# Kernel tuning notes

Hardware: AMD Instinct MI355X
Metric: run time of the kernel (lower is better)

The kernel has to match this reference:

```python
import jax, jax.numpy as jnp
import numpy as np

N = 50000
E = 800000
NUM_GRAPHS = 64
D_IN = 261
D_SAGE = 64
D_LIN = 32
N_SAGE_REST = 6
N_LIN_REST = 3
EPS = 1e-5


def _layernorm(x, g, b):
    mu = jnp.mean(x, axis=-1, keepdims=True)
    var = jnp.mean((x - mu) ** 2, axis=-1, keepdims=True)
    return (x - mu) * jax.lax.rsqrt(var + EPS) * g + b


def _sage_block(x, Wl, bl, Wr, g, b, src, dst, inv_deg, residual):
    # mean aggregation of neighbor (source) features onto targets
    msum = jax.ops.segment_sum(x[src], dst, num_segments=N)  # [N, d]
    mean = msum * inv_deg  # [N, d]
    f = mean @ Wl + bl + x @ Wr  # lin_l(aggr) + lin_r(x); lin_r has no bias
    f = jax.nn.gelu(f, approximate=False)
    f = _layernorm(f, g, b)
    if residual:
        f = f + x
    return f


def _lin_block(x, W, b, g, beta, residual):
    f = jax.nn.gelu(x @ W + b, approximate=False)
    f = _layernorm(f, g, beta)
    if residual:
        f = f + x
    return f


def setup_inputs() -> dict:
    key = jax.random.key(0)
    ks = jax.random.split(key, 24)
    x = jax.random.normal(ks[0], (N, D_IN), dtype=jnp.float32)
    edge_index = jax.random.randint(ks[1], (2, E), 0, N, dtype=jnp.int64)
    batch = jnp.sort(jax.random.randint(ks[2], (N,), 0, NUM_GRAPHS, dtype=jnp.int64))

    def glorot(k, shape):
        fan_in = shape[0]
        return jax.random.normal(k, shape, dtype=jnp.float32) / np.sqrt(fan_in)

    inp = {
        "x": x, "edge_index": edge_index, "batch": batch,
        # first SAGE block (261 -> 64, no residual)
        "Wl0": glorot(ks[3], (D_IN, D_SAGE)), "bl0": jnp.zeros((D_SAGE,), jnp.float32),
        "Wr0": glorot(ks[4], (D_IN, D_SAGE)),
        "g0": jnp.ones((D_SAGE,), jnp.float32), "beta0": jnp.zeros((D_SAGE,), jnp.float32),
        # 6 residual SAGE blocks (64 -> 64), stacked
        "Wl": glorot(ks[5], (N_SAGE_REST, D_SAGE, D_SAGE)),
        "bl": jnp.zeros((N_SAGE_REST, D_SAGE), jnp.float32),
        "Wr": glorot(ks[6], (N_SAGE_REST, D_SAGE, D_SAGE)),
        "g": jnp.ones((N_SAGE_REST, D_SAGE), jnp.float32),
        "beta": jnp.zeros((N_SAGE_REST, D_SAGE), jnp.float32),
        # MLP: first LinearBlock 64 -> 32 (no residual)
        "M0": glorot(ks[7], (D_SAGE, D_LIN)), "mb0": jnp.zeros((D_LIN,), jnp.float32),
        "mg0": jnp.ones((D_LIN,), jnp.float32), "mbeta0": jnp.zeros((D_LIN,), jnp.float32),
        # 3 residual LinearBlocks 32 -> 32, stacked
        "M": glorot(ks[8], (N_LIN_REST, D_LIN, D_LIN)),
        "mb": jnp.zeros((N_LIN_REST, D_LIN), jnp.float32),
        "mg": jnp.ones((N_LIN_REST, D_LIN), jnp.float32),
        "mbeta": jnp.zeros((N_LIN_REST, D_LIN), jnp.float32),
        # final Linear 32 -> 1
        "Wf": glorot(ks[9], (D_LIN, 1)), "bf": jnp.zeros((1,), jnp.float32),
    }
    return inp


def reference(x, edge_index, batch, Wl0, bl0, Wr0, g0, beta0, Wl, bl, Wr, g, beta,
              M0, mb0, mg0, mbeta0, M, mb, mg, mbeta, Wf, bf):
    src, dst = edge_index[0], edge_index[1]
    deg = jax.ops.segment_sum(jnp.ones((E,), x.dtype), dst, num_segments=N)
    inv_deg = (1.0 / jnp.maximum(deg, 1.0))[:, None]  # [N,1]

    h = _sage_block(x, Wl0, bl0, Wr0, g0, beta0, src, dst, inv_deg, residual=False)
    for i in range(N_SAGE_REST):
        h = _sage_block(h, Wl[i], bl[i], Wr[i], g[i], beta[i], src, dst, inv_deg, residual=True)

    pooled = jax.ops.segment_sum(h, batch, num_segments=NUM_GRAPHS)  # [G, 64]

    m = _lin_block(pooled, M0, mb0, mg0, mbeta0, residual=False)
    for i in range(N_LIN_REST):
        m = _lin_block(m, M[i], mb[i], mg[i], mbeta[i], residual=True)
    return m @ Wf + bf  # [G, 1]
```

## Files before the change

### kernel.cpp

```cpp
#include <hip/hip_runtime.h>
#include <hip/hip_bf16.h>
#include <math.h>

#define N_NODES 50000
#define N_EDGES 800000
#define NUM_GRAPHS 64
#define NPAD 50048
#define KPAD0 288
#define PSPLIT 16
#define MAXDEG 64

#define GEMM0_GRID (NPAD / 64)
#define SCAT_GRID  ((N_EDGES + 255) / 256)
#define ZERO_GRID  ((N_NODES + 255) / 256)
#define PREPW_TOT  (128 * KPAD0 + 6 * 128 * 64)
#define PREPW_GRID ((PREPW_TOT + 255) / 256)

typedef __attribute__((ext_vector_type(8))) short short8;
typedef __attribute__((ext_vector_type(4))) float f32x4;

__device__ __forceinline__ float gelu_f(float v) {
    return 0.5f * v * (1.0f + erff(v * 0.70710678118654752440f));
}

__device__ __forceinline__ float half_sum32(float v) {
    v += __shfl_xor(v, 1); v += __shfl_xor(v, 2); v += __shfl_xor(v, 4);
    v += __shfl_xor(v, 8); v += __shfl_xor(v, 16);
    return v;
}

__device__ __forceinline__ float group_sum8(float v) {
    v += __shfl_xor(v, 1); v += __shfl_xor(v, 2); v += __shfl_xor(v, 4);
    return v;
}

__device__ __forceinline__ unsigned short f2bf(float f) {
    unsigned int u = __float_as_uint(f);
    unsigned int r = (u + 0x7fffu + ((u >> 16) & 1u)) >> 16;
    return (unsigned short)r;
}

__device__ __forceinline__ float bf_lo(unsigned int u) {
    return __uint_as_float(u << 16);
}
__device__ __forceinline__ float bf_hi(unsigned int u) {
    return __uint_as_float(u & 0xffff0000u);
}


__global__ void k_prep(int* __restrict__ deg,
                       const float* __restrict__ Wl0, const float* __restrict__ Wr0,
                       const float* __restrict__ Wl, const float* __restrict__ Wr,
                       unsigned short* __restrict__ Bt0, unsigned short* __restrict__ BtR) {
    const int blk = blockIdx.x, tid = threadIdx.x;
    if (blk < ZERO_GRID) {
        int i = blk * 256 + tid;
        if (i < N_NODES) deg[i] = 0;
        return;
    }
    int idx = (blk - ZERO_GRID) * 256 + tid;
    const int n0 = 128 * KPAD0;
    if (idx < n0) {
        int j = idx / KPAD0, k = idx - j * KPAD0;
        float v = 0.0f;
        if (k < 261) v = (j < 64) ? Wl0[k * 64 + j] : Wr0[k * 64 + (j - 64)];
        Bt0[idx] = f2bf(v);
    } else if (idx < PREPW_TOT) {
        int r = idx - n0;
        int l = r >> 13;
        int rr = r & 8191;
        int j = rr >> 6, k = rr & 63;
        float v = (j < 64) ? Wl[l * 4096 + k * 64 + j] : Wr[l * 4096 + k * 64 + (j - 64)];
        BtR[r] = f2bf(v);
    }
}


__global__ __launch_bounds__(256) void k_front(
        const float* __restrict__ X, const unsigned short* __restrict__ Bt0,
        unsigned short* __restrict__ U, float* __restrict__ V,
        const int* __restrict__ src, const int* __restrict__ dst,
        int* __restrict__ deg, unsigned short* __restrict__ col64) {
    __shared__ __align__(16) unsigned short sA[64 * 32];
    __shared__ __align__(16) unsigned short sB[128 * 32];
    const int blk = blockIdx.x;
    const int tid = threadIdx.x;

    if (blk < GEMM0_GRID) {
        const int lane = tid & 63, wid = tid >> 6;
        const int l16 = lane & 15, quad = lane >> 4;
        const int m0 = blk * 64;
        f32x4 acc[8];
        #pragma unroll
        for (int j = 0; j < 8; ++j) { acc[j][0] = 0.f; acc[j][1] = 0.f; acc[j][2] = 0.f; acc[j][3] = 0.f; }
        const int arow = tid >> 2, apart = (tid & 3) << 3;
        const int node = m0 + arow;
        const int rowok = (node < N_NODES);
        for (int kc = 0; kc < KPAD0; kc += 32) {
            if (kc) __syncthreads();
            short8 av;
            #pragma unroll
            for (int j = 0; j < 8; ++j) {
                int kk = kc + apart + j;
                float val = (rowok && kk < 261) ? X[(size_t)node * 261 + kk] : 0.0f;
                av[j] = (short)f2bf(val);
            }
            *(short8*)&sA[arow * 32 + apart] = av;
            #pragma unroll
            for (int q = 0; q < 2; ++q) {
                int flat = q * 256 + tid;
                int br = flat >> 2, bp = (flat & 3) << 3;
                *(int4*)&sB[br * 32 + bp] = *(const int4*)&Bt0[(size_t)br * KPAD0 + kc + bp];
            }
            __syncthreads();
            short8 af = *(const short8*)&sA[(wid * 16 + l16) * 32 + quad * 8];
            #pragma unroll
            for (int j = 0; j < 8; ++j) {
                short8 bf = *(const short8*)&sB[(j * 16 + l16) * 32 + quad * 8];
                acc[j] = __builtin_amdgcn_mfma_f32_16x16x32_bf16(af, bf, acc[j], 0, 0, 0);
            }
        }
        const int rbase = m0 + wid * 16 + quad * 4;
        #pragma unroll
        for (int j = 0; j < 4; ++j)
            #pragma unroll
            for (int r = 0; r < 4; ++r)
                U[(size_t)(rbase + r) * 64 + j * 16 + l16] = f2bf(acc[j][r]);
        #pragma unroll
        for (int j = 4; j < 8; ++j)
            #pragma unroll
            for (int r = 0; r < 4; ++r)
                V[(size_t)(rbase + r) * 64 + (j - 4) * 16 + l16] = acc[j][r];
    } else {
        int i = (blk - GEMM0_GRID) * 256 + tid;
        if (i < N_EDGES) {
            int d = dst[i];
            int pos = atomicAdd(&deg[d], 1);
            if (pos < MAXDEG) col64[(d << 6) + pos] = (unsigned short)src[i];
        }
    }
}


__global__ __launch_bounds__(256) void k_mgemm(const unsigned short* __restrict__ A, int Kpad,
                                               const unsigned short* __restrict__ Bt,
                                               unsigned short* __restrict__ U, float* __restrict__ V) {
    __shared__ __align__(16) unsigned short sA[64 * 32];
    __shared__ __align__(16) unsigned short sB[128 * 32];
    const int tid = threadIdx.x;
    const int lane = tid & 63, wid = tid >> 6;
    const int l16 = lane & 15, quad = lane >> 4;
    const int m0 = blockIdx.x * 64;

    f32x4 acc[8];
    #pragma unroll
    for (int j = 0; j < 8; ++j) { acc[j][0] = 0.f; acc[j][1] = 0.f; acc[j][2] = 0.f; acc[j][3] = 0.f; }

    const int arow = tid >> 2, apart = (tid & 3) << 3;
    for (int kc = 0; kc < Kpad; kc += 32) {
        if (kc) __syncthreads();
        *(int4*)&sA[arow * 32 + apart] = *(const int4*)&A[(size_t)(m0 + arow) * Kpad + kc + apart];
        #pragma unroll
        for (int q = 0; q < 2; ++q) {
            int flat = q * 256 + tid;
            int br = flat >> 2, bp = (flat & 3) << 3;
            *(int4*)&sB[br * 32 + bp] = *(const int4*)&Bt[(size_t)br * Kpad + kc + bp];
        }
        __syncthreads();
        short8 af = *(const short8*)&sA[(wid * 16 + l16) * 32 + quad * 8];
        #pragma unroll
        for (int j = 0; j < 8; ++j) {
            short8 bf = *(const short8*)&sB[(j * 16 + l16) * 32 + quad * 8];
            acc[j] = __builtin_amdgcn_mfma_f32_16x16x32_bf16(af, bf, acc[j], 0, 0, 0);
        }
    }
    const int rbase = m0 + wid * 16 + quad * 4;
    #pragma unroll
    for (int j = 0; j < 4; ++j)
        #pragma unroll
        for (int r = 0; r < 4; ++r)
            U[(size_t)(rbase + r) * 64 + j * 16 + l16] = f2bf(acc[j][r]);
    #pragma unroll
    for (int j = 4; j < 8; ++j)
        #pragma unroll
        for (int r = 0; r < 4; ++r)
            V[(size_t)(rbase + r) * 64 + (j - 4) * 16 + l16] = acc[j][r];
}


__global__ __launch_bounds__(256) void k_aggln(const unsigned short* __restrict__ U, const float* Vv,
                                               const unsigned short* __restrict__ h_in,
                                               unsigned short* __restrict__ h_out, float* hf_out,
                                               const int* __restrict__ deg,
                                               const unsigned short* __restrict__ col64,
                                               const float* __restrict__ bias, const float* __restrict__ gam,
                                               const float* __restrict__ bet, int n, int residual) {
    const int lane = threadIdx.x & 63, wid = threadIdx.x >> 6;
    const int sub = lane >> 3, hl = lane & 7;
    const int base = lane & 56;
    const int node = blockIdx.x * 32 + wid * 8 + sub;
    const bool valid = (node < n);
    const int nd = valid ? node : 0;
    const int dg = valid ? deg[nd] : 0;
    const int cnt = min(dg, MAXDEG);
    uint4 cv = make_uint4(0u, 0u, 0u, 0u);
    if (valid) cv = *(const uint4*)&col64[((size_t)nd << 6) + hl * 8];
    const uint4* __restrict__ Up = (const uint4*)U;
    float s0 = 0.f, s1 = 0.f, s2 = 0.f, s3 = 0.f, s4 = 0.f, s5 = 0.f, s6 = 0.f, s7 = 0.f;
    for (int b = 0; b * 8 < cnt; b += 2) {
        #pragma unroll
        for (int h = 0; h < 2; ++h) {
            const int sl = base + b + h;
            unsigned int p0 = (unsigned int)__shfl((int)cv.x, sl);
            unsigned int p1 = (unsigned int)__shfl((int)cv.y, sl);
            unsigned int p2 = (unsigned int)__shfl((int)cv.z, sl);
            unsigned int p3 = (unsigned int)__shfl((int)cv.w, sl);
            const int eb = (b + h) * 8;
            int c[8];
            c[0] = (int)(p0 & 0xffffu); c[1] = (int)(p0 >> 16);
            c[2] = (int)(p1 & 0xffffu); c[3] = (int)(p1 >> 16);
            c[4] = (int)(p2 & 0xffffu); c[5] = (int)(p2 >> 16);
            c[6] = (int)(p3 & 0xffffu); c[7] = (int)(p3 >> 16);
            #pragma unroll
            for (int i = 0; i < 8; ++i) {
                uint4 u = (eb + i < cnt) ? Up[(size_t)c[i] * 8 + hl] : make_uint4(0u, 0u, 0u, 0u);
                s0 += bf_lo(u.x); s1 += bf_hi(u.x);
                s2 += bf_lo(u.y); s3 += bf_hi(u.y);
                s4 += bf_lo(u.z); s5 += bf_hi(u.z);
                s6 += bf_lo(u.w); s7 += bf_hi(u.w);
            }
        }
    }
    const float id = 1.0f / fmaxf((float)dg, 1.0f);
    const float4 b0 = *(const float4*)&bias[8 * hl];
    const float4 b1 = *(const float4*)&bias[8 * hl + 4];
    float4 v0 = make_float4(0.f, 0.f, 0.f, 0.f), v1 = v0;
    if (valid) {
        v0 = *(const float4*)&Vv[(size_t)nd * 64 + 8 * hl];
        v1 = *(const float4*)&Vv[(size_t)nd * 64 + 8 * hl + 4];
    }
    float f0 = gelu_f(s0 * id + b0.x + v0.x);
    float f1 = gelu_f(s1 * id + b0.y + v0.y);
    float f2 = gelu_f(s2 * id + b0.z + v0.z);
    float f3 = gelu_f(s3 * id + b0.w + v0.w);
    float f4 = gelu_f(s4 * id + b1.x + v1.x);
    float f5 = gelu_f(s5 * id + b1.y + v1.y);
    float f6 = gelu_f(s6 * id + b1.z + v1.z);
    float f7 = gelu_f(s7 * id + b1.w + v1.w);
    float mu = group_sum8(((f0 + f1) + (f2 + f3)) + ((f4 + f5) + (f6 + f7))) * 0.015625f;
    float d0 = f0 - mu, d1 = f1 - mu, d2 = f2 - mu, d3 = f3 - mu;
    float d4 = f4 - mu, d5 = f5 - mu, d6 = f6 - mu, d7 = f7 - mu;
    float var = group_sum8(((d0 * d0 + d1 * d1) + (d2 * d2 + d3 * d3)) +
                           ((d4 * d4 + d5 * d5) + (d6 * d6 + d7 * d7))) * 0.015625f;
    float rs = rsqrtf(var + 1e-5f);
    const float4 g0v = *(const float4*)&gam[8 * hl];
    const float4 g1v = *(const float4*)&gam[8 * hl + 4];
    const float4 e0v = *(const float4*)&bet[8 * hl];
    const float4 e1v = *(const float4*)&bet[8 * hl + 4];
    f0 = d0 * rs * g0v.x + e0v.x;
    f1 = d1 * rs * g0v.y + e0v.y;
    f2 = d2 * rs * g0v.z + e0v.z;
    f3 = d3 * rs * g0v.w + e0v.w;
    f4 = d4 * rs * g1v.x + e1v.x;
    f5 = d5 * rs * g1v.y + e1v.y;
    f6 = d6 * rs * g1v.z + e1v.z;
    f7 = d7 * rs * g1v.w + e1v.w;
    if (residual && valid) {
        uint4 hu = ((const uint4*)h_in)[(size_t)nd * 8 + hl];
        f0 += bf_lo(hu.x); f1 += bf_hi(hu.x);
        f2 += bf_lo(hu.y); f3 += bf_hi(hu.y);
        f4 += bf_lo(hu.z); f5 += bf_hi(hu.z);
        f6 += bf_lo(hu.w); f7 += bf_hi(hu.w);
    }
    if (valid) {
        uint4 outw;
        outw.x = (unsigned int)f2bf(f0) | ((unsigned int)f2bf(f1) << 16);
        outw.y = (unsigned int)f2bf(f2) | ((unsigned int)f2bf(f3) << 16);
        outw.z = (unsigned int)f2bf(f4) | ((unsigned int)f2bf(f5) << 16);
        outw.w = (unsigned int)f2bf(f6) | ((unsigned int)f2bf(f7) << 16);
        ((uint4*)h_out)[(size_t)nd * 8 + hl] = outw;
        if (hf_out) {
            *(float4*)&hf_out[(size_t)nd * 64 + 8 * hl] = make_float4(f0, f1, f2, f3);
            *(float4*)&hf_out[(size_t)nd * 64 + 8 * hl + 4] = make_float4(f4, f5, f6, f7);
        }
    }
}


__global__ __launch_bounds__(256) void k_pool1(const float* __restrict__ h, const int* __restrict__ batch,
                                               float* __restrict__ partial, int n) {
    __shared__ float sred[4][64];
    const int g = blockIdx.x / PSPLIT;
    const int s = blockIdx.x - g * PSPLIT;
    const int lane = threadIdx.x & 63, wid = threadIdx.x >> 6;
    int lo = 0, hi = n;
    while (lo < hi) { int mid = (lo + hi) >> 1; if (batch[mid] < g) lo = mid + 1; else hi = mid; }
    const int start = lo;
    lo = 0; hi = n;
    while (lo < hi) { int mid = (lo + hi) >> 1; if (batch[mid] < g + 1) lo = mid + 1; else hi = mid; }
    const int end = lo;
    const int len = end - start;
    const int chunk = (len + PSPLIT - 1) / PSPLIT;
    const int a = start + s * chunk;
    const int b = min(a + chunk, end);
    float sum = 0.0f;
    for (int node = a + wid; node < b; node += 4) sum += h[(size_t)node * 64 + lane];
    sred[wid][lane] = sum;
    __syncthreads();
    if (wid == 0)
        partial[(size_t)blockIdx.x * 64 + lane] = sred[0][lane] + sred[1][lane] + sred[2][lane] + sred[3][lane];
}


__global__ __launch_bounds__(1024) void k_head(const float* __restrict__ partial,
                                               const float* __restrict__ M0, const float* __restrict__ mb0,
                                               const float* __restrict__ mg0, const float* __restrict__ mbeta0,
                                               const float* __restrict__ M, const float* __restrict__ mb,
                                               const float* __restrict__ mg, const float* __restrict__ mbeta,
                                               const float* __restrict__ Wf, const float* __restrict__ bf,
                                               float* __restrict__ out) {
    __shared__ float sP[64 * 64];
    __shared__ float sA[64 * 33];
    __shared__ float sB[64 * 33];
    const int tx = threadIdx.x, ty = threadIdx.y;
    const int tid = ty * 32 + tx;
    for (int i = tid; i < 64 * 64; i += 1024) {
        int g = i >> 6, f = i & 63;
        float s = 0.0f;
        #pragma unroll
        for (int s2 = 0; s2 < PSPLIT; ++s2) s += partial[(size_t)(g * PSPLIT + s2) * 64 + f];
        sP[i] = s;
    }
    __syncthreads();
    #pragma unroll
    for (int rr = 0; rr < 2; ++rr) {
        int r = ty + rr * 32;
        float a = mb0[tx];
        for (int k = 0; k < 64; ++k) a += sP[r * 64 + k] * M0[k * 32 + tx];
        a = gelu_f(a);
        float mu = half_sum32(a) * (1.0f / 32.0f);
        float d = a - mu;
        float var = half_sum32(d * d) * (1.0f / 32.0f);
        a = d * rsqrtf(var + 1e-5f) * mg0[tx] + mbeta0[tx];
        sA[r * 33 + tx] = a;
    }
    __syncthreads();
    float* cur = sA;
    float* nxt = sB;
    for (int L = 0; L < 3; ++L) {
        const float* Mi = M + L * 32 * 32;
        const float* mbi = mb + L * 32;
        const float* mgi = mg + L * 32;
        const float* mbetai = mbeta + L * 32;
        #pragma unroll
        for (int rr = 0; rr < 2; ++rr) {
            int r = ty + rr * 32;
            float a = mbi[tx];
            for (int k = 0; k < 32; ++k) a += cur[r * 33 + k] * Mi[k * 32 + tx];
            a = gelu_f(a);
            float mu = half_sum32(a) * (1.0f / 32.0f);
            float d = a - mu;
            float var = half_sum32(d * d) * (1.0f / 32.0f);
            a = d * rsqrtf(var + 1e-5f) * mgi[tx] + mbetai[tx] + cur[r * 33 + tx];
            nxt[r * 33 + tx] = a;
        }
        __syncthreads();
        float* t = cur; cur = nxt; nxt = t;
    }
    #pragma unroll
    for (int rr = 0; rr < 2; ++rr) {
        int r = ty + rr * 32;
        float p = cur[r * 33 + tx] * Wf[tx];
        p = half_sum32(p);
        if (tx == 0) out[r] = p + bf[0];
    }
}


extern "C" void kernel_launch(void* const* d_in, const int* in_sizes, int n_in,
                              void* d_out, int out_size, void* d_ws, size_t ws_size,
                              hipStream_t stream) {
    const int N = N_NODES;
    const int E = N_EDGES;

    const float* x    = (const float*)d_in[0];
    const int* eidx   = (const int*)d_in[1];
    const int* batch  = (const int*)d_in[2];
    const float* Wl0  = (const float*)d_in[3];
    const float* bl0  = (const float*)d_in[4];
    const float* Wr0  = (const float*)d_in[5];
    const float* g0   = (const float*)d_in[6];
    const float* bet0 = (const float*)d_in[7];
    const float* Wl   = (const float*)d_in[8];
    const float* bl   = (const float*)d_in[9];
    const float* Wr   = (const float*)d_in[10];
    const float* gR   = (const float*)d_in[11];
    const float* betR = (const float*)d_in[12];
    const float* M0   = (const float*)d_in[13];
    const float* mb0  = (const float*)d_in[14];
    const float* mg0  = (const float*)d_in[15];
    const float* mbe0 = (const float*)d_in[16];
    const float* M    = (const float*)d_in[17];
    const float* mb   = (const float*)d_in[18];
    const float* mg   = (const float*)d_in[19];
    const float* mbe  = (const float*)d_in[20];
    const float* Wf   = (const float*)d_in[21];
    const float* bf   = (const float*)d_in[22];

    const int* src = eidx;
    const int* dst = eidx + E;

    char* p = (char*)d_ws;
    auto alloc = [&](size_t bytes) -> void* {
        void* q = (void*)p;
        p += (bytes + 255) & ~(size_t)255;
        return q;
    };
    int*   deg    = (int*)alloc((size_t)N * 4);
    unsigned short* col64 = (unsigned short*)alloc((size_t)N * MAXDEG * 2);
    unsigned short* Bt0 = (unsigned short*)alloc((size_t)128 * KPAD0 * 2);
    unsigned short* BtR = (unsigned short*)alloc((size_t)6 * 128 * 64 * 2);
    unsigned short* U   = (unsigned short*)alloc((size_t)NPAD * 64 * 2);
    float* V    = (float*)alloc((size_t)NPAD * 64 * 4);
    float* partial = (float*)alloc((size_t)NUM_GRAPHS * PSPLIT * 64 * 4);
    unsigned short* hbfA = (unsigned short*)alloc((size_t)NPAD * 64 * 2);
    unsigned short* hbfB = (unsigned short*)alloc((size_t)NPAD * 64 * 2);

    k_prep<<<ZERO_GRID + PREPW_GRID, 256, 0, stream>>>(deg, Wl0, Wr0, Wl, Wr, Bt0, BtR);

    k_front<<<GEMM0_GRID + SCAT_GRID, 256, 0, stream>>>(
        x, Bt0, U, V, src, dst, deg, col64);

    const int gemm_grid = NPAD / 64;
    const int agg_grid = (N + 31) / 32;

    k_aggln<<<agg_grid, 256, 0, stream>>>(U, V, nullptr, hbfA, nullptr, deg, col64,
                                          bl0, g0, bet0, N, 0);

    unsigned short* hin = hbfA;
    unsigned short* hout = hbfB;
    for (int i = 0; i < 6; ++i) {
        k_mgemm<<<gemm_grid, 256, 0, stream>>>(hin, 64, BtR + (size_t)i * 128 * 64, U, V);
        k_aggln<<<agg_grid, 256, 0, stream>>>(U, V, hin, hout, (i == 5) ? V : nullptr,
                                              deg, col64,
                                              bl + (size_t)i * 64, gR + (size_t)i * 64,
                                              betR + (size_t)i * 64, N, 1);
        unsigned short* t = hin; hin = hout; hout = t;
    }

    k_pool1<<<NUM_GRAPHS * PSPLIT, 256, 0, stream>>>(V, batch, partial, N);
    k_head<<<1, dim3(32, 32), 0, stream>>>(partial, M0, mb0, mg0, mbe0, M, mb, mg, mbe, Wf, bf, (float*)d_out);
}
```

Measured before the change: 416.1 us.

## Fuse aggregation/LayerNorm with next layer's dense GEMM into one per-layer kernel

Merges the neighbor-aggregation+GELU+LayerNorm kernel with the following layer's MFMA GEMM. Each block processes 64 nodes, writes the bf16 output rows into shared memory and immediately multiplies them by the next layer's weights, avoiding a global reload of h and one launch per layer. U/V buffers are now double-buffered and h is updated in place. The cost is fewer concurrent nodes per aggregation block, larger LDS use, and a block-wide barrier between the gather and GEMM phases.

New measurement: 405.9 us. 2.4% less time.

```diff
diff --git a/kernel.cpp b/kernel.cpp
--- a/kernel.cpp
+++ b/kernel.cpp
@@ -142,148 +142,149 @@
 }
 
 
-__global__ __launch_bounds__(256) void k_mgemm(const unsigned short* __restrict__ A, int Kpad,
-                                               const unsigned short* __restrict__ Bt,
-                                               unsigned short* __restrict__ U, float* __restrict__ V) {
-    __shared__ __align__(16) unsigned short sA[64 * 32];
+__global__ __launch_bounds__(256) void k_layer(
+        const unsigned short* __restrict__ U_in, const float* __restrict__ V_in,
+        unsigned short* __restrict__ h,
+        float* __restrict__ hf_out,
+        const int* __restrict__ deg, const unsigned short* __restrict__ col64,
+        const float* __restrict__ bias, const float* __restrict__ gam,
+        const float* __restrict__ bet,
+        const unsigned short* __restrict__ Bt_next,
+        unsigned short* __restrict__ U_out, float* __restrict__ V_out,
+        int residual, int have_gemm) {
+    __shared__ __align__(16) unsigned short sA[2 * 64 * 32];
     __shared__ __align__(16) unsigned short sB[128 * 32];
     const int tid = threadIdx.x;
     const int lane = tid & 63, wid = tid >> 6;
-    const int l16 = lane & 15, quad = lane >> 4;
-    const int m0 = blockIdx.x * 64;
-
-    f32x4 acc[8];
-    #pragma unroll
-    for (int j = 0; j < 8; ++j) { acc[j][0] = 0.f; acc[j][1] = 0.f; acc[j][2] = 0.f; acc[j][3] = 0.f; }
-
-    const int arow = tid >> 2, apart = (tid & 3) << 3;
-    for (int kc = 0; kc < Kpad; kc += 32) {
-        if (kc) __syncthreads();
-        *(int4*)&sA[arow * 32 + apart] = *(const int4*)&A[(size_t)(m0 + arow) * Kpad + kc + apart];
-        #pragma unroll
-        for (int q = 0; q < 2; ++q) {
-            int flat = q * 256 + tid;
-            int br = flat >> 2, bp = (flat & 3) << 3;
-            *(int4*)&sB[br * 32 + bp] = *(const int4*)&Bt[(size_t)br * Kpad + kc + bp];
-        }
-        __syncthreads();
-        short8 af = *(const short8*)&sA[(wid * 16 + l16) * 32 + quad * 8];
-        #pragma unroll
-        for (int j = 0; j < 8; ++j) {
-            short8 bf = *(const short8*)&sB[(j * 16 + l16) * 32 + quad * 8];
-            acc[j] = __builtin_amdgcn_mfma_f32_16x16x32_bf16(af, bf, acc[j], 0, 0, 0);
-        }
-    }
-    const int rbase = m0 + wid * 16 + quad * 4;
-    #pragma unroll
-    for (int j = 0; j < 4; ++j)
-        #pragma unroll
-        for (int r = 0; r < 4; ++r)
-            U[(size_t)(rbase + r) * 64 + j * 16 + l16] = f2bf(acc[j][r]);
-    #pragma unroll
-    for (int j = 4; j < 8; ++j)
-        #pragma unroll
-        for (int r = 0; r < 4; ++r)
-            V[(size_t)(rbase + r) * 64 + (j - 4) * 16 + l16] = acc[j][r];
-}
-
-
-__global__ __launch_bounds__(256) void k_aggln(const unsigned short* __restrict__ U, const float* Vv,
-                                               const unsigned short* __restrict__ h_in,
-                                               unsigned short* __restrict__ h_out, float* hf_out,
-                                               const int* __restrict__ deg,
-                                               const unsigned short* __restrict__ col64,
-                                               const float* __restrict__ bias, const float* __restrict__ gam,
-                                               const float* __restrict__ bet, int n, int residual) {
-    const int lane = threadIdx.x & 63, wid = threadIdx.x >> 6;
     const int sub = lane >> 3, hl = lane & 7;
     const int base = lane & 56;
-    const int node = blockIdx.x * 32 + wid * 8 + sub;
-    const bool valid = (node < n);
-    const int nd = valid ? node : 0;
-    const int dg = valid ? deg[nd] : 0;
-    const int cnt = min(dg, MAXDEG);
-    uint4 cv = make_uint4(0u, 0u, 0u, 0u);
-    if (valid) cv = *(const uint4*)&col64[((size_t)nd << 6) + hl * 8];
-    const uint4* __restrict__ Up = (const uint4*)U;
-    float s0 = 0.f, s1 = 0.f, s2 = 0.f, s3 = 0.f, s4 = 0.f, s5 = 0.f, s6 = 0.f, s7 = 0.f;
-    for (int b = 0; b * 8 < cnt; b += 2) {
-        #pragma unroll
-        for (int h = 0; h < 2; ++h) {
-            const int sl = base + b + h;
-            unsigned int p0 = (unsigned int)__shfl((int)cv.x, sl);
-            unsigned int p1 = (unsigned int)__shfl((int)cv.y, sl);
-            unsigned int p2 = (unsigned int)__shfl((int)cv.z, sl);
-            unsigned int p3 = (unsigned int)__shfl((int)cv.w, sl);
-            const int eb = (b + h) * 8;
-            int c[8];
-            c[0] = (int)(p0 & 0xffffu); c[1] = (int)(p0 >> 16);
-            c[2] = (int)(p1 & 0xffffu); c[3] = (int)(p1 >> 16);
-            c[4] = (int)(p2 & 0xffffu); c[5] = (int)(p2 >> 16);
-            c[6] = (int)(p3 & 0xffffu); c[7] = (int)(p3 >> 16);
-            #pragma unroll
-            for (int i = 0; i < 8; ++i) {
-                uint4 u = (eb + i < cnt) ? Up[(size_t)c[i] * 8 + hl] : make_uint4(0u, 0u, 0u, 0u);
-                s0 += bf_lo(u.x); s1 += bf_hi(u.x);
-                s2 += bf_lo(u.y); s3 += bf_hi(u.y);
-                s4 += bf_lo(u.z); s5 += bf_hi(u.z);
-                s6 += bf_lo(u.w); s7 += bf_hi(u.w);
+    const int m0 = blockIdx.x * 64;
+    const uint4* __restrict__ Up = (const uint4*)U_in;
+
+    #pragma unroll
+    for (int rep = 0; rep < 2; ++rep) {
+        const int nl = rep * 32 + wid * 8 + sub;
+        const int node = m0 + nl;
+        const bool valid = (node < N_NODES);
+        const int nd = valid ? node : 0;
+        const int dg = valid ? deg[nd] : 0;
+        const int cnt = min(dg, MAXDEG);
+        uint4 cv = make_uint4(0u, 0u, 0u, 0u);
+        if (valid) cv = *(const uint4*)&col64[((size_t)nd << 6) + hl * 8];
+        float s0 = 0.f, s1 = 0.f, s2 = 0.f, s3 = 0.f, s4 = 0.f, s5 = 0.f, s6 = 0.f, s7 = 0.f;
+        for (int b = 0; b * 8 < cnt; b += 2) {
+            #pragma unroll
+            for (int hh = 0; hh < 2; ++hh) {
+                const int sl = base + b + hh;
+                unsigned int p0 = (unsigned int)__shfl((int)cv.x, sl);
+                unsigned int p1 = (unsigned int)__shfl((int)cv.y, sl);
+                unsigned int p2 = (unsigned int)__shfl((int)cv.z, sl);
+                unsigned int p3 = (unsigned int)__shfl((int)cv.w, sl);
+                const int eb = (b + hh) * 8;
+                int c[8];
+                c[0] = (int)(p0 & 0xffffu); c[1] = (int)(p0 >> 16);
+                c[2] = (int)(p1 & 0xffffu); c[3] = (int)(p1 >> 16);
+                c[4] = (int)(p2 & 0xffffu); c[5] = (int)(p2 >> 16);
+                c[6] = (int)(p3 & 0xffffu); c[7] = (int)(p3 >> 16);
+                #pragma unroll
+                for (int i = 0; i < 8; ++i) {
+                    uint4 u = (eb + i < cnt) ? Up[(size_t)c[i] * 8 + hl] : make_uint4(0u, 0u, 0u, 0u);
+                    s0 += bf_lo(u.x); s1 += bf_hi(u.x);
+                    s2 += bf_lo(u.y); s3 += bf_hi(u.y);
+                    s4 += bf_lo(u.z); s5 += bf_hi(u.z);
+                    s6 += bf_lo(u.w); s7 += bf_hi(u.w);
+                }
             }
         }
-    }
-    const float id = 1.0f / fmaxf((float)dg, 1.0f);
-    const float4 b0 = *(const float4*)&bias[8 * hl];
-    const float4 b1 = *(const float4*)&bias[8 * hl + 4];
-    float4 v0 = make_float4(0.f, 0.f, 0.f, 0.f), v1 = v0;
-    if (valid) {
-        v0 = *(const float4*)&Vv[(size_t)nd * 64 + 8 * hl];
-        v1 = *(const float4*)&Vv[(size_t)nd * 64 + 8 * hl + 4];
-    }
-    float f0 = gelu_f(s0 * id + b0.x + v0.x);
-    float f1 = gelu_f(s1 * id + b0.y + v0.y);
-    float f2 = gelu_f(s2 * id + b0.z + v0.z);
-    float f3 = gelu_f(s3 * id + b0.w + v0.w);
-    float f4 = gelu_f(s4 * id + b1.x + v1.x);
-    float f5 = gelu_f(s5 * id + b1.y + v1.y);
-    float f6 = gelu_f(s6 * id + b1.z + v1.z);
-    float f7 = gelu_f(s7 * id + b1.w + v1.w);
-    float mu = group_sum8(((f0 + f1) + (f2 + f3)) + ((f4 + f5) + (f6 + f7))) * 0.015625f;
-    float d0 = f0 - mu, d1 = f1 - mu, d2 = f2 - mu, d3 = f3 - mu;
-    float d4 = f4 - mu, d5 = f5 - mu, d6 = f6 - mu, d7 = f7 - mu;
-    float var = group_sum8(((d0 * d0 + d1 * d1) + (d2 * d2 + d3 * d3)) +
-                           ((d4 * d4 + d5 * d5) + (d6 * d6 + d7 * d7))) * 0.015625f;
-    float rs = rsqrtf(var + 1e-5f);
-    const float4 g0v = *(const float4*)&gam[8 * hl];
-    const float4 g1v = *(const float4*)&gam[8 * hl + 4];
-    const float4 e0v = *(const float4*)&bet[8 * hl];
-    const float4 e1v = *(const float4*)&bet[8 * hl + 4];
-    f0 = d0 * rs * g0v.x + e0v.x;
-    f1 = d1 * rs * g0v.y + e0v.y;
-    f2 = d2 * rs * g0v.z + e0v.z;
-    f3 = d3 * rs * g0v.w + e0v.w;
-    f4 = d4 * rs * g1v.x + e1v.x;
-    f5 = d5 * rs * g1v.y + e1v.y;
-    f6 = d6 * rs * g1v.z + e1v.z;
-    f7 = d7 * rs * g1v.w + e1v.w;
-    if (residual && valid) {
-        uint4 hu = ((const uint4*)h_in)[(size_t)nd * 8 + hl];
-        f0 += bf_lo(hu.x); f1 += bf_hi(hu.x);
-        f2 += bf_lo(hu.y); f3 += bf_hi(hu.y);
-        f4 += bf_lo(hu.z); f5 += bf_hi(hu.z);
-        f6 += bf_lo(hu.w); f7 += bf_hi(hu.w);
-    }
-    if (valid) {
+        const float id = 1.0f / fmaxf((float)dg, 1.0f);
+        const float4 b0 = *(const float4*)&bias[8 * hl];
+        const float4 b1 = *(const float4*)&bias[8 * hl + 4];
+        float4 v0 = make_float4(0.f, 0.f, 0.f, 0.f), v1 = v0;
+        if (valid) {
+            v0 = *(const float4*)&V_in[(size_t)nd * 64 + 8 * hl];
+            v1 = *(const float4*)&V_in[(size_t)nd * 64 + 8 * hl + 4];
+        }
+        float f0 = gelu_f(s0 * id + b0.x + v0.x);
+        float f1 = gelu_f(s1 * id + b0.y + v0.y);
+        float f2 = gelu_f(s2 * id + b0.z + v0.z);
+        float f3 = gelu_f(s3 * id + b0.w + v0.w);
+        float f4 = gelu_f(s4 * id + b1.x + v1.x);
+        float f5 = gelu_f(s5 * id + b1.y + v1.y);
+        float f6 = gelu_f(s6 * id + b1.z + v1.z);
+        float f7 = gelu_f(s7 * id + b1.w + v1.w);
+        float mu = group_sum8(((f0 + f1) + (f2 + f3)) + ((f4 + f5) + (f6 + f7))) * 0.015625f;
+        float d0 = f0 - mu, d1 = f1 - mu, d2 = f2 - mu, d3 = f3 - mu;
+        float d4 = f4 - mu, d5 = f5 - mu, d6 = f6 - mu, d7 = f7 - mu;
+        float var = group_sum8(((d0 * d0 + d1 * d1) + (d2 * d2 + d3 * d3)) +
+                               ((d4 * d4 + d5 * d5) + (d6 * d6 + d7 * d7))) * 0.015625f;
+        float rs = rsqrtf(var + 1e-5f);
+        const float4 g0v = *(const float4*)&gam[8 * hl];
+        const float4 g1v = *(const float4*)&gam[8 * hl + 4];
+        const float4 e0v = *(const float4*)&bet[8 * hl];
+        const float4 e1v = *(const float4*)&bet[8 * hl + 4];
+        f0 = d0 * rs * g0v.x + e0v.x;
+        f1 = d1 * rs * g0v.y + e0v.y;
+        f2 = d2 * rs * g0v.z + e0v.z;
+        f3 = d3 * rs * g0v.w + e0v.w;
+        f4 = d4 * rs * g1v.x + e1v.x;
+        f5 = d5 * rs * g1v.y + e1v.y;
+        f6 = d6 * rs * g1v.z + e1v.z;
+        f7 = d7 * rs * g1v.w + e1v.w;
+        if (residual && valid) {
+            uint4 hu = ((const uint4*)h)[(size_t)nd * 8 + hl];
+            f0 += bf_lo(hu.x); f1 += bf_hi(hu.x);
+            f2 += bf_lo(hu.y); f3 += bf_hi(hu.y);
+            f4 += bf_lo(hu.z); f5 += bf_hi(hu.z);
+            f6 += bf_lo(hu.w); f7 += bf_hi(hu.w);
+        }
         uint4 outw;
         outw.x = (unsigned int)f2bf(f0) | ((unsigned int)f2bf(f1) << 16);
         outw.y = (unsigned int)f2bf(f2) | ((unsigned int)f2bf(f3) << 16);
         outw.z = (unsigned int)f2bf(f4) | ((unsigned int)f2bf(f5) << 16);
         outw.w = (unsigned int)f2bf(f6) | ((unsigned int)f2bf(f7) << 16);
-        ((uint4*)h_out)[(size_t)nd * 8 + hl] = outw;
-        if (hf_out) {
-            *(float4*)&hf_out[(size_t)nd * 64 + 8 * hl] = make_float4(f0, f1, f2, f3);
-            *(float4*)&hf_out[(size_t)nd * 64 + 8 * hl + 4] = make_float4(f4, f5, f6, f7);
-        }
-    }
+        if (valid) {
+            ((uint4*)h)[(size_t)nd * 8 + hl] = outw;
+            if (hf_out) {
+                *(float4*)&hf_out[(size_t)nd * 64 + 8 * hl] = make_float4(f0, f1, f2, f3);
+                *(float4*)&hf_out[(size_t)nd * 64 + 8 * hl + 4] = make_float4(f4, f5, f6, f7);
+            }
+        }
+        *(uint4*)&sA[(((hl >> 2) * 64 + nl) << 5) + (hl & 3) * 8] = outw;
+    }
+    if (!have_gemm) return;
+    __syncthreads();
+
+    const int l16 = lane & 15, quad = lane >> 4;
+    f32x4 acc[8];
+    #pragma unroll
+    for (int j = 0; j < 8; ++j) { acc[j][0] = 0.f; acc[j][1] = 0.f; acc[j][2] = 0.f; acc[j][3] = 0.f; }
+    for (int kc = 0; kc < 64; kc += 32) {
+        if (kc) __syncthreads();
+        #pragma unroll
+        for (int q = 0; q < 2; ++q) {
+            int flat = q * 256 + tid;
+            int br = flat >> 2, bp = (flat & 3) << 3;
+            *(int4*)&sB[br * 32 + bp] = *(const int4*)&Bt_next[(size_t)br * 64 + kc + bp];
+        }
+        __syncthreads();
+        short8 af = *(const short8*)&sA[(((kc >> 5) * 64 + wid * 16 + l16) << 5) + quad * 8];
+        #pragma unroll
+        for (int j = 0; j < 8; ++j) {
+            short8 bf = *(const short8*)&sB[(j * 16 + l16) * 32 + quad * 8];
+            acc[j] = __builtin_amdgcn_mfma_f32_16x16x32_bf16(af, bf, acc[j], 0, 0, 0);
+        }
+    }
+    const int rbase = m0 + wid * 16 + quad * 4;
+    #pragma unroll
+    for (int j = 0; j < 4; ++j)
+        #pragma unroll
+        for (int r = 0; r < 4; ++r)
+            U_out[(size_t)(rbase + r) * 64 + j * 16 + l16] = f2bf(acc[j][r]);
+    #pragma unroll
+    for (int j = 4; j < 8; ++j)
+        #pragma unroll
+        for (int r = 0; r < 4; ++r)
+            V_out[(size_t)(rbase + r) * 64 + (j - 4) * 16 + l16] = acc[j][r];
 }
 
 
@@ -420,34 +421,35 @@
     unsigned short* col64 = (unsigned short*)alloc((size_t)N * MAXDEG * 2);
     unsigned short* Bt0 = (unsigned short*)alloc((size_t)128 * KPAD0 * 2);
     unsigned short* BtR = (unsigned short*)alloc((size_t)6 * 128 * 64 * 2);
-    unsigned short* U   = (unsigned short*)alloc((size_t)NPAD * 64 * 2);
-    float* V    = (float*)alloc((size_t)NPAD * 64 * 4);
+    unsigned short* Ua  = (unsigned short*)alloc((size_t)NPAD * 64 * 2);
+    unsigned short* Ub  = (unsigned short*)alloc((size_t)NPAD * 64 * 2);
+    float* Va   = (float*)alloc((size_t)NPAD * 64 * 4);
+    float* Vb   = (float*)alloc((size_t)NPAD * 64 * 4);
+    unsigned short* hbuf = (unsigned short*)alloc((size_t)NPAD * 64 * 2);
     float* partial = (float*)alloc((size_t)NUM_GRAPHS * PSPLIT * 64 * 4);
-    unsigned short* hbfA = (unsigned short*)alloc((size_t)NPAD * 64 * 2);
-    unsigned short* hbfB = (unsigned short*)alloc((size_t)NPAD * 64 * 2);
 
     k_prep<<<ZERO_GRID + PREPW_GRID, 256, 0, stream>>>(deg, Wl0, Wr0, Wl, Wr, Bt0, BtR);
 
     k_front<<<GEMM0_GRID + SCAT_GRID, 256, 0, stream>>>(
-        x, Bt0, U, V, src, dst, deg, col64);
-
-    const int gemm_grid = NPAD / 64;
-    const int agg_grid = (N + 31) / 32;
-
-    k_aggln<<<agg_grid, 256, 0, stream>>>(U, V, nullptr, hbfA, nullptr, deg, col64,
-                                          bl0, g0, bet0, N, 0);
-
-    unsigned short* hin = hbfA;
-    unsigned short* hout = hbfB;
-    for (int i = 0; i < 6; ++i) {
-        k_mgemm<<<gemm_grid, 256, 0, stream>>>(hin, 64, BtR + (size_t)i * 128 * 64, U, V);
-        k_aggln<<<agg_grid, 256, 0, stream>>>(U, V, hin, hout, (i == 5) ? V : nullptr,
-                                              deg, col64,
-                                              bl + (size_t)i * 64, gR + (size_t)i * 64,
-                                              betR + (size_t)i * 64, N, 1);
-        unsigned short* t = hin; hin = hout; hout = t;
-    }
-
-    k_pool1<<<NUM_GRAPHS * PSPLIT, 256, 0, stream>>>(V, batch, partial, N);
+        x, Bt0, Ua, Va, src, dst, deg, col64);
+
+    unsigned short* Uin = Ua;  float* Vin = Va;
+    unsigned short* Uout = Ub; float* Vout = Vb;
+    for (int i = 0; i < 7; ++i) {
+        const float* bias = (i == 0) ? bl0  : bl  + (size_t)(i - 1) * 64;
+        const float* gam  = (i == 0) ? g0   : gR  + (size_t)(i - 1) * 64;
+        const float* bet  = (i == 0) ? bet0 : betR + (size_t)(i - 1) * 64;
+        const int have_gemm = (i < 6);
+        float* hf = (i == 6) ? Vout : nullptr;
+        k_layer<<<GEMM0_GRID, 256, 0, stream>>>(
+            Uin, Vin, hbuf, hf, deg, col64, bias, gam, bet,
+            have_gemm ? (BtR + (size_t)i * 128 * 64) : BtR,
+            Uout, Vout, (i > 0) ? 1 : 0, have_gemm);
+        unsigned short* tu = Uin; Uin = Uout; Uout = tu;
+        float* tv = Vin; Vin = Vout; Vout = tv;
+    }
+    float* hf_final = Vin;
+
+    k_pool1<<<NUM_GRAPHS * PSPLIT, 256, 0, stream>>>(hf_final, batch, partial, N);
     k_head<<<1, dim3(32, 32), 0, stream>>>(partial, M0, mb0, mg0, mbe0, M, mb, mg, mbe, Wf, bf, (float*)d_out);
 }
```
